# Performance work log

Measured on AMD Instinct MI355X. Metric: run time of the kernel, lower is better.

Reference implementation:

```python
import jax, jax.numpy as jnp
import numpy as np
import math

# ---- static config (mirrors init_kwargs) ----
B, CIN, COUT = 8, 32, 32
H, W = 256, 256
RADIUS_CUTOFF = 0.03
NR, NPHI = 6, 7               # kernel_shape = [6, 7] (anisotropic basis)
K = (NR - 1) * NPHI + 1       # 36 basis functions
EPS = 1e-5                    # InstanceNorm2d eps
NEG_SLOPE = 0.2


def _disco_psi(nh, nw, r_cutoff, nr, nphi):
    """Local DISCO filter basis on an equidistant [-1,1]^2 grid.
    Returns psi [K, P, P] (float32) and half-width p (P = 2p+1).
    Piecewise-linear hat functions in radius (nr rings incl. center) times
    hat functions in angle (nphi sectors), normalized and quadrature-weighted."""
    dy = 2.0 / nh
    dx = 2.0 / nw
    p = int(math.floor(r_cutoff / min(dx, dy)))
    off_y = (np.arange(-p, p + 1) * dy)[:, None]
    off_x = (np.arange(-p, p + 1) * dx)[None, :]
    r = np.sqrt(off_x ** 2 + off_y ** 2)                 # [P, P]
    phi = np.arctan2(off_y + 0 * off_x, off_x + 0 * off_y) % (2.0 * np.pi)
    dr = r_cutoff / nr
    dphi = 2.0 * np.pi / nphi
    ker = (nr - 1) * nphi + 1
    ik = np.arange(ker)[:, None, None]                   # [K,1,1]
    ir = ((ik - 1) // nphi + 1) * dr                     # ik=0 -> ring at r=0
    iphi = ((ik - 1) % nphi) * dphi
    norm = np.pi * (r_cutoff * nr / (nr + 1)) ** 2       # 2d normalization
    rv = np.clip(1.0 - np.abs(r[None] - ir) / dr, 0.0, None) * (r[None] <= r_cutoff)
    dphi_abs = np.abs(phi[None] - iphi)
    dphi_min = np.minimum(dphi_abs, 2.0 * np.pi - dphi_abs)
    pv = np.where(ik > 0, np.clip(1.0 - dphi_min / dphi, 0.0, None), 1.0)
    q = dx * dy                                          # quadrature weight
    psi = (rv * pv) * (q / norm)
    return jnp.asarray(psi, jnp.float32), p


def _upsample2x_bilinear_align_corners(x):
    """torch nn.Upsample(scale_factor=2, mode='bilinear', align_corners=True)."""
    b, c, hi, wi = x.shape
    ho, wo = 2 * hi, 2 * wi
    ys = jnp.linspace(0.0, hi - 1.0, ho)
    y0 = jnp.clip(jnp.floor(ys), 0, hi - 2).astype(jnp.int32)
    wy = (ys - y0.astype(ys.dtype))[None, None, :, None]
    x = x[:, :, y0, :] * (1.0 - wy) + x[:, :, y0 + 1, :] * wy
    xs = jnp.linspace(0.0, wi - 1.0, wo)
    x0 = jnp.clip(jnp.floor(xs), 0, wi - 2).astype(jnp.int32)
    wx = (xs - x0.astype(xs.dtype))[None, None, None, :]
    return x[:, :, :, x0] * (1.0 - wx) + x[:, :, :, x0 + 1] * wx


def setup_inputs() -> dict:
    key = jax.random.key(0)
    k1, k2 = jax.random.split(key)
    image = jax.random.normal(k1, (B, CIN, H, W), dtype=jnp.float32)
    # DISCO learnable weights: [out_ch, in_ch, kernel_size]
    scale = 1.0 / np.sqrt(CIN * K)
    weight = jax.random.normal(k2, (COUT, CIN, K), dtype=jnp.float32) * scale
    return {"image": image, "weight": weight}


def reference(image, weight):
    x = _upsample2x_bilinear_align_corners(image)
    # 2) equidistant DISCO conv: assemble dense kernel from basis, strided conv back to (H,W)
    psi, p = _disco_psi(2 * H, 2 * W, RADIUS_CUTOFF / 2.0, NR, NPHI)   # [K,P,P]
    kernel = jnp.einsum("oik,kyx->oiyx", weight, psi)                   # [O,I,P,P]
    y = jax.lax.conv_general_dilated(
        x, kernel, window_strides=(2, 2), padding=[(p, p), (p, p)],
        dimension_numbers=("NCHW", "OIHW", "NCHW"))                     # [B,O,H,W]
    # 3) InstanceNorm2d (no affine), biased variance over spatial dims
    mean = jnp.mean(y, axis=(2, 3), keepdims=True)
    var = jnp.var(y, axis=(2, 3), keepdims=True)
    y = (y - mean) * jax.lax.rsqrt(var + EPS)
    # 4) LeakyReLU(0.2)
    return jnp.where(y >= 0, y, NEG_SLOPE * y)
```

## Files before the change

### kernel.cpp

```cpp
#include <hip/hip_runtime.h>
#include <hip/hip_bf16.h>
#include <math.h>

#define B_     8
#define CIN_   32
#define COUT_  32
#define H_     256
#define W_     256
#define K_     36
#define P_     3
#define KW_    7
#define TAPS_  49
#define NPAIR_ 25
#define EPS_   1e-5f
#define SLOPE_ 0.2f

#define PART_OFF_F   25600
#define MEANRS_OFF_F 156672

#define IMG_PLANE_B   6736
#define IMG_ROW_B     336

#define XP_ROW   304
#define XO_BASE  11552

using short8_t  = __attribute__((ext_vector_type(8)))  short;
using f32x16_t  = __attribute__((ext_vector_type(16))) float;
using f32x4_t   = __attribute__((ext_vector_type(4)))  float;

__device__ inline ushort f32_to_bf16(float f) {
    unsigned int bits = __float_as_uint(f);
    unsigned int r = (bits + 0x7FFFu + ((bits >> 16) & 1u)) >> 16;
    return (ushort)r;
}

__host__ __device__ inline int pair_tap(int pi, int tt) {
    if (pi < 21) {
        const int ky = pi / 3, c = pi % 3;
        return ky * 7 + 2 * c + tt;
    }
    const int row = 2 * (pi - 21) + tt;
    return (row <= 6) ? (row * 7 + 6) : -1;
}

__global__ __launch_bounds__(256)
void build_kernel(const float* __restrict__ weight, ushort* __restrict__ kerB) {
    __shared__ float psi_s[2][K_];
    const int f  = blockIdx.x;
    const int pi = f % NPAIR_;
    const int oc = f / NPAIR_;
    const int tid = threadIdx.x;

    if (tid < 2 * K_) {
        const int tt = tid / K_;
        const int k  = tid - tt * K_;
        const int tap = pair_tap(pi, tt);
        float val = 0.f;
        if (tap >= 0) {
            const int ky = tap / 7;
            const int kx = tap % 7;
            const double dxy   = 2.0 / 512.0;
            const double rcut  = 0.015;
            const int    nr    = 6, nphi = 7;
            const double dr    = rcut / nr;
            const double dphi  = 2.0 * M_PI / nphi;
            const double norm  = M_PI * (rcut * nr / (nr + 1)) * (rcut * nr / (nr + 1));
            const double q     = dxy * dxy;
            const double offy = (double)(ky - P_) * dxy;
            const double offx = (double)(kx - P_) * dxy;
            const double r    = sqrt(offx * offx + offy * offy);
            double phi = atan2(offy, offx);
            if (phi < 0.0) phi += 2.0 * M_PI;
            double ir, iphi;
            if (k == 0) { ir = 0.0; iphi = 0.0; }
            else        { ir = (double)((k - 1) / nphi + 1) * dr;
                          iphi = (double)((k - 1) % nphi) * dphi; }
            double rv = 1.0 - fabs(r - ir) / dr;
            rv = rv > 0.0 ? rv : 0.0;
            if (r > rcut) rv = 0.0;
            double pv = 1.0;
            if (k > 0) {
                double da = fabs(phi - iphi);
                double dm = da < (2.0 * M_PI - da) ? da : (2.0 * M_PI - da);
                pv = 1.0 - dm / dphi;
                pv = pv > 0.0 ? pv : 0.0;
            }
            val = (float)(rv * pv * q / norm);
        }
        psi_s[tt][k] = val;
    }
    __syncthreads();

    for (int e = tid; e < 512; e += 256) {
        const int lane = e >> 3;
        const int j    = e & 7;
        const int gs   = lane >> 5;
        const int n    = lane & 31;
        float s = 0.f;
        if (pair_tap(pi, gs) >= 0) {
            const int ci = oc * 8 + j;
            const float* w = weight + (size_t)(n * CIN_ + ci) * K_;
            #pragma unroll
            for (int k = 0; k < K_; ++k) s = fmaf(w[k], psi_s[gs][k], s);
        }
        kerB[((size_t)f * 64 + lane) * 8 + j] = f32_to_bf16(s);
    }
}

__global__ __launch_bounds__(512, 8)
void conv_mfma(const float* __restrict__ image,
               const ushort* __restrict__ kerB,
               float* __restrict__ out,
               float* __restrict__ partials) {
    __shared__ float  Img_s[3368];
    __shared__ ushort Xup_s[11552];
    __shared__ float  wp[8][32][2];

    const int tid  = threadIdx.x;
    const int lane = tid & 63;
    const int w    = tid >> 6;
    const int j0 = blockIdx.x * 16;
    const int i0 = blockIdx.y * 16;
    const int b  = blockIdx.z;

    const int u0 = 2 * i0 - 3;
    const int v0 = 2 * j0 - 3;
    const int R0 = i0 - 2;
    const int C0 = j0 - 2;

    const int gs  = lane >> 5;
    const int tio = (lane & 31) >> 4;
    const int tj  = lane & 15;
    const int yb0 = 4 * w + 2 * tio;

    f32x16_t acc;
    #pragma unroll
    for (int q = 0; q < 16; ++q) acc[q] = 0.f;

    char* img_bytes = (char*)Img_s;
    char* xup_bytes = (char*)Xup_s;

    if (tid < 19) {
        const short8_t z = {0,0,0,0,0,0,0,0};
        *(short8_t*)(xup_bytes + 37 * XP_ROW + tid * 16) = z;
    }

    const float* imgb = image + (size_t)(b * CIN_) * (H_ * W_);

    for (int oc = 0; oc < 4; ++oc) {
        const float* img = imgb + (size_t)(oc * 8) * (H_ * W_);
        for (int e = tid; e < 800; e += 512) {
            const int p  = (e >= 400) ? 1 : 0;
            const int yx = e - p * 400;
            const int py = yx / 20, px = yx - py * 20;
            const int row = R0 + py, col = C0 + px;
            f32x4_t g = {0.f, 0.f, 0.f, 0.f};
            if ((unsigned)row < 256u && (unsigned)col < 256u) {
                const float* q = img + (size_t)p * 4 * (H_ * W_) + row * W_ + col;
                g[0] = q[0];
                g[1] = q[H_ * W_];
                g[2] = q[2 * (H_ * W_)];
                g[3] = q[3 * (H_ * W_)];
            }
            *(f32x4_t*)(img_bytes + p * IMG_PLANE_B + (py * 21 + px) * 16) = g;
        }
        __syncthreads();

        for (int e = tid; e < 703; e += 512) {
            const int y   = e / 19;
            const int xp  = e - 19 * y;
            const int x   = 2 * xp;
            const int ry  = y >> 1;
            const float wy =
                (float)((((y & 1) ? 510 : 255)) - (R0 + ry)) * (1.0f / 511.0f);
            const int Ax = C0 + xp;
            const float wx0 = (float)(255 - Ax) * (1.0f / 511.0f);
            const float wx1 = (float)(510 - Ax) * (1.0f / 511.0f);
            const bool oky = ((unsigned)(u0 + y) < 512u);
            const bool ok0 = oky && ((unsigned)(v0 + x) < 512u);
            const bool ok1 = oky && ((unsigned)(v0 + x + 1) < 512u) && (xp < 18);

            const char* lo = img_bytes + (ry * 21 + xp) * 16;
            const char* hi = lo + IMG_PLANE_B;
            const f32x4_t a00 = *(const f32x4_t*)(lo);
            const f32x4_t a01 = *(const f32x4_t*)(lo + 16);
            const f32x4_t a10 = *(const f32x4_t*)(lo + IMG_ROW_B);
            const f32x4_t a11 = *(const f32x4_t*)(lo + IMG_ROW_B + 16);
            const f32x4_t b00 = *(const f32x4_t*)(hi);
            const f32x4_t b01 = *(const f32x4_t*)(hi + 16);
            const f32x4_t b10 = *(const f32x4_t*)(hi + IMG_ROW_B);
            const f32x4_t b11 = *(const f32x4_t*)(hi + IMG_ROW_B + 16);

            const f32x4_t cA0 = a00 + wy * (a10 - a00);
            const f32x4_t cA1 = a01 + wy * (a11 - a01);
            const f32x4_t cB0 = b00 + wy * (b10 - b00);
            const f32x4_t cB1 = b01 + wy * (b11 - b01);

            {
                const f32x4_t va = cA0 + wx0 * (cA1 - cA0);
                const f32x4_t vb = cB0 + wx0 * (cB1 - cB0);
                __hip_bfloat162 h0 = __float22bfloat162_rn(make_float2(va[0], va[1]));
                __hip_bfloat162 h1 = __float22bfloat162_rn(make_float2(va[2], va[3]));
                __hip_bfloat162 h2 = __float22bfloat162_rn(make_float2(vb[0], vb[1]));
                __hip_bfloat162 h3 = __float22bfloat162_rn(make_float2(vb[2], vb[3]));
                union { short8_t s8; uint4 u4; } pk;
                pk.u4.x = ok0 ? *(unsigned int*)&h0 : 0u;
                pk.u4.y = ok0 ? *(unsigned int*)&h1 : 0u;
                pk.u4.z = ok0 ? *(unsigned int*)&h2 : 0u;
                pk.u4.w = ok0 ? *(unsigned int*)&h3 : 0u;
                *(short8_t*)(xup_bytes + y * XP_ROW + xp * 16) = pk.s8;
            }
            {
                const f32x4_t va = cA0 + wx1 * (cA1 - cA0);
                const f32x4_t vb = cB0 + wx1 * (cB1 - cB0);
                __hip_bfloat162 h0 = __float22bfloat162_rn(make_float2(va[0], va[1]));
                __hip_bfloat162 h1 = __float22bfloat162_rn(make_float2(va[2], va[3]));
                __hip_bfloat162 h2 = __float22bfloat162_rn(make_float2(vb[0], vb[1]));
                __hip_bfloat162 h3 = __float22bfloat162_rn(make_float2(vb[2], vb[3]));
                union { short8_t s8; uint4 u4; } pk;
                pk.u4.x = ok1 ? *(unsigned int*)&h0 : 0u;
                pk.u4.y = ok1 ? *(unsigned int*)&h1 : 0u;
                pk.u4.z = ok1 ? *(unsigned int*)&h2 : 0u;
                pk.u4.w = ok1 ? *(unsigned int*)&h3 : 0u;
                *(short8_t*)(xup_bytes + XO_BASE + y * XP_ROW + xp * 16) = pk.s8;
            }
        }
        __syncthreads();

        const ushort* kbp = kerB + ((size_t)(oc * NPAIR_) * 64 + lane) * 8;
        const int baseA = (gs ? XO_BASE : 0) + yb0 * XP_ROW + tj * 16;
        const int baseB = (yb0 + gs) * XP_ROW + (tj + 3) * 16;

        #pragma unroll
        for (int ky = 0; ky < KW_; ++ky) {
            short8_t bf0 = *(const short8_t*)(kbp + (size_t)((ky * 3 + 0) * 512));
            short8_t bf1 = *(const short8_t*)(kbp + (size_t)((ky * 3 + 1) * 512));
            short8_t bf2 = *(const short8_t*)(kbp + (size_t)((ky * 3 + 2) * 512));
            const int rbase = baseA + ky * XP_ROW;
            const short8_t a0 = *(const short8_t*)(xup_bytes + rbase);
            acc = __builtin_amdgcn_mfma_f32_32x32x16_bf16(a0, bf0, acc, 0, 0, 0);
            const short8_t a1 = *(const short8_t*)(xup_bytes + rbase + 16);
            acc = __builtin_amdgcn_mfma_f32_32x32x16_bf16(a1, bf1, acc, 0, 0, 0);
            const short8_t a2 = *(const short8_t*)(xup_bytes + rbase + 32);
            acc = __builtin_amdgcn_mfma_f32_32x32x16_bf16(a2, bf2, acc, 0, 0, 0);
        }
        #pragma unroll
        for (int q = 0; q < 4; ++q) {
            const short8_t bfq =
                *(const short8_t*)(kbp + (size_t)((21 + q) * 512));
            const short8_t aq =
                *(const short8_t*)(xup_bytes + baseB + q * (2 * XP_ROW));
            acc = __builtin_amdgcn_mfma_f32_32x32x16_bf16(aq, bfq, acc, 0, 0, 0);
        }
        __syncthreads();
    }

    const int n = lane & 31;
    float* op = out + (size_t)(b * COUT_ + n) * (H_ * W_);
    const int ibase = i0 + 2 * w;
    #pragma unroll
    for (int grp = 0; grp < 4; ++grp) {
        const int ti  = ibase + (grp >> 1);
        const int tjj = j0 + ((grp & 1) ? 8 : 0) + 4 * gs;
        f32x4_t s;
        s[0] = acc[grp * 4 + 0]; s[1] = acc[grp * 4 + 1];
        s[2] = acc[grp * 4 + 2]; s[3] = acc[grp * 4 + 3];
        *(f32x4_t*)(op + (size_t)ti * W_ + tjj) = s;
    }

    float s1 = 0.f, s2 = 0.f;
    #pragma unroll
    for (int q = 0; q < 16; ++q) { s1 += acc[q]; s2 = fmaf(acc[q], acc[q], s2); }
    s1 += __shfl_xor(s1, 32);
    s2 += __shfl_xor(s2, 32);
    if (lane < 32) { wp[w][lane][0] = s1; wp[w][lane][1] = s2; }
    __syncthreads();
    if (tid < 32) {
        float t1 = 0.f, t2 = 0.f;
        #pragma unroll
        for (int wv = 0; wv < 8; ++wv) { t1 += wp[wv][tid][0]; t2 += wp[wv][tid][1]; }
        const int tile = blockIdx.y * 16 + blockIdx.x;
        float2* pp = (float2*)partials;
        pp[((b * 32 + tid) << 8) | tile] = make_float2(t1, t2);
    }
}

__global__ __launch_bounds__(64)
void stats_kernel(const float* __restrict__ partials, float* __restrict__ meanrs) {
    const int bo = blockIdx.x;
    const int l  = threadIdx.x;
    const float2* pp = (const float2*)partials + ((size_t)bo << 8);
    float s1 = 0.f, s2 = 0.f;
    #pragma unroll
    for (int k = 0; k < 4; ++k) {
        const float2 p = pp[l + 64 * k];
        s1 += p.x; s2 += p.y;
    }
    #pragma unroll
    for (int off = 32; off > 0; off >>= 1) {
        s1 += __shfl_down(s1, off);
        s2 += __shfl_down(s2, off);
    }
    if (l == 0) {
        const float inv = 1.0f / 65536.0f;
        const float m   = s1 * inv;
        const float var = s2 * inv - m * m;
        ((float2*)meanrs)[bo] = make_float2(m, 1.0f / sqrtf(var + EPS_));
    }
}

__global__ __launch_bounds__(256)
void norm2_kernel(float* __restrict__ y, const float* __restrict__ meanrs) {
    const int blk = blockIdx.x;
    const int bo  = blk >> 6;
    const float2 mr = ((const float2*)meanrs)[bo];
    const float m  = mr.x;
    const float rs = mr.y;

    const int e = blk * 256 + threadIdx.x;
    float4 v = ((const float4*)y)[e];
    v.x = (v.x - m) * rs; v.x = v.x >= 0.f ? v.x : SLOPE_ * v.x;
    v.y = (v.y - m) * rs; v.y = v.y >= 0.f ? v.y : SLOPE_ * v.y;
    v.z = (v.z - m) * rs; v.z = v.z >= 0.f ? v.z : SLOPE_ * v.z;
    v.w = (v.w - m) * rs; v.w = v.w >= 0.f ? v.w : SLOPE_ * v.w;
    ((float4*)y)[e] = v;
}

extern "C" void kernel_launch(void* const* d_in, const int* in_sizes, int n_in,
                              void* d_out, int out_size, void* d_ws, size_t ws_size,
                              hipStream_t stream) {
    const float* image  = (const float*)d_in[0];
    const float* weight = (const float*)d_in[1];
    float*  out      = (float*)d_out;
    ushort* kerB     = (ushort*)d_ws;
    float*  partials = (float*)d_ws + PART_OFF_F;
    float*  meanrs   = (float*)d_ws + MEANRS_OFF_F;

    build_kernel<<<dim3(4 * NPAIR_), dim3(256), 0, stream>>>(weight, kerB);
    conv_mfma<<<dim3(16, 16, B_), dim3(512), 0, stream>>>(image, kerB, out, partials);
    stats_kernel<<<dim3(256), dim3(64), 0, stream>>>(partials, meanrs);
    norm2_kernel<<<dim3(16384), dim3(256), 0, stream>>>(out, meanrs);
}
```

Measured before the change: 116.8 us.

## Fuse image staging into upsample by reading global memory directly

Removes the shared-memory staging buffer for the input tile. Each thread now loads its four bilinear neighbours straight from global memory, with clamped indices, and writes bf16 upsampled values into the Xup buffer. The work is split per plane half, giving 1406 items instead of 703. This drops one barrier per channel group and the LDS footprint, which could raise occupancy. In exchange, each input pixel is fetched several times from global or L2 memory with scattered 4-byte loads.

```diff
diff --git a/kernel.cpp b/kernel.cpp
--- a/kernel.cpp
+++ b/kernel.cpp
@@ -17,9 +17,6 @@
 
 #define PART_OFF_F   25600
 #define MEANRS_OFF_F 156672
-
-#define IMG_PLANE_B   6736
-#define IMG_ROW_B     336
 
 #define XP_ROW   304
 #define XO_BASE  11552
@@ -112,7 +109,6 @@
                const ushort* __restrict__ kerB,
                float* __restrict__ out,
                float* __restrict__ partials) {
-    __shared__ float  Img_s[3368];
     __shared__ ushort Xup_s[11552];
     __shared__ float  wp[8][32][2];
 
@@ -137,93 +133,68 @@
     #pragma unroll
     for (int q = 0; q < 16; ++q) acc[q] = 0.f;
 
-    char* img_bytes = (char*)Img_s;
     char* xup_bytes = (char*)Xup_s;
 
     if (tid < 19) {
         const short8_t z = {0,0,0,0,0,0,0,0};
         *(short8_t*)(xup_bytes + 37 * XP_ROW + tid * 16) = z;
     }
+    __syncthreads();
 
     const float* imgb = image + (size_t)(b * CIN_) * (H_ * W_);
 
     for (int oc = 0; oc < 4; ++oc) {
-        const float* img = imgb + (size_t)(oc * 8) * (H_ * W_);
-        for (int e = tid; e < 800; e += 512) {
-            const int p  = (e >= 400) ? 1 : 0;
-            const int yx = e - p * 400;
-            const int py = yx / 20, px = yx - py * 20;
-            const int row = R0 + py, col = C0 + px;
-            f32x4_t g = {0.f, 0.f, 0.f, 0.f};
-            if ((unsigned)row < 256u && (unsigned)col < 256u) {
-                const float* q = img + (size_t)p * 4 * (H_ * W_) + row * W_ + col;
-                g[0] = q[0];
-                g[1] = q[H_ * W_];
-                g[2] = q[2 * (H_ * W_)];
-                g[3] = q[3 * (H_ * W_)];
+        for (int e = tid; e < 1406; e += 512) {
+            const int item = e >> 1;
+            const int p    = e & 1;
+            const int y    = item / 19;
+            const int xp   = item - 19 * y;
+            const int ry   = y >> 1;
+            const int r0   = R0 + ry;
+            const int c0   = C0 + xp;
+            const float wy  = (float)(((y & 1) ? 510 : 255) - r0) * (1.0f / 511.0f);
+            const float wx0 = (float)(255 - c0) * (1.0f / 511.0f);
+            const float wx1 = (float)(510 - c0) * (1.0f / 511.0f);
+            const bool oky = ((unsigned)(u0 + y) < 512u);
+            const bool ok0 = oky && ((unsigned)(v0 + 2 * xp) < 512u);
+            const bool ok1 = oky && ((unsigned)(v0 + 2 * xp + 1) < 512u) && (xp < 18);
+
+            const int r0c = r0 < 0 ? 0 : (r0 > 255 ? 255 : r0);
+            const int r1t = r0 + 1;
+            const int r1c = r1t < 0 ? 0 : (r1t > 255 ? 255 : r1t);
+            const int c0c = c0 < 0 ? 0 : (c0 > 255 ? 255 : c0);
+            const int c1t = c0 + 1;
+            const int c1c = c1t < 0 ? 0 : (c1t > 255 ? 255 : c1t);
+
+            const float* pl = imgb + (size_t)(oc * 8 + p * 4) * (H_ * W_);
+            const int o00 = r0c * W_ + c0c, o01 = r0c * W_ + c1c;
+            const int o10 = r1c * W_ + c0c, o11 = r1c * W_ + c1c;
+
+            float ve[4], vo[4];
+            #pragma unroll
+            for (int c = 0; c < 4; ++c) {
+                const float* q = pl + (size_t)c * (H_ * W_);
+                const float v00 = q[o00];
+                const float v01 = q[o01];
+                const float v10 = q[o10];
+                const float v11 = q[o11];
+                const float l0 = v00 + wy * (v10 - v00);
+                const float l1 = v01 + wy * (v11 - v01);
+                ve[c] = l0 + wx0 * (l1 - l0);
+                vo[c] = l0 + wx1 * (l1 - l0);
             }
-            *(f32x4_t*)(img_bytes + p * IMG_PLANE_B + (py * 21 + px) * 16) = g;
-        }
-        __syncthreads();
-
-        for (int e = tid; e < 703; e += 512) {
-            const int y   = e / 19;
-            const int xp  = e - 19 * y;
-            const int x   = 2 * xp;
-            const int ry  = y >> 1;
-            const float wy =
-                (float)((((y & 1) ? 510 : 255)) - (R0 + ry)) * (1.0f / 511.0f);
-            const int Ax = C0 + xp;
-            const float wx0 = (float)(255 - Ax) * (1.0f / 511.0f);
-            const float wx1 = (float)(510 - Ax) * (1.0f / 511.0f);
-            const bool oky = ((unsigned)(u0 + y) < 512u);
-            const bool ok0 = oky && ((unsigned)(v0 + x) < 512u);
-            const bool ok1 = oky && ((unsigned)(v0 + x + 1) < 512u) && (xp < 18);
-
-            const char* lo = img_bytes + (ry * 21 + xp) * 16;
-            const char* hi = lo + IMG_PLANE_B;
-            const f32x4_t a00 = *(const f32x4_t*)(lo);
-            const f32x4_t a01 = *(const f32x4_t*)(lo + 16);
-            const f32x4_t a10 = *(const f32x4_t*)(lo + IMG_ROW_B);
-            const f32x4_t a11 = *(const f32x4_t*)(lo + IMG_ROW_B + 16);
-            const f32x4_t b00 = *(const f32x4_t*)(hi);
-            const f32x4_t b01 = *(const f32x4_t*)(hi + 16);
-            const f32x4_t b10 = *(const f32x4_t*)(hi + IMG_ROW_B);
-            const f32x4_t b11 = *(const f32x4_t*)(hi + IMG_ROW_B + 16);
-
-            const f32x4_t cA0 = a00 + wy * (a10 - a00);
-            const f32x4_t cA1 = a01 + wy * (a11 - a01);
-            const f32x4_t cB0 = b00 + wy * (b10 - b00);
-            const f32x4_t cB1 = b01 + wy * (b11 - b01);
-
-            {
-                const f32x4_t va = cA0 + wx0 * (cA1 - cA0);
-                const f32x4_t vb = cB0 + wx0 * (cB1 - cB0);
-                __hip_bfloat162 h0 = __float22bfloat162_rn(make_float2(va[0], va[1]));
-                __hip_bfloat162 h1 = __float22bfloat162_rn(make_float2(va[2], va[3]));
-                __hip_bfloat162 h2 = __float22bfloat162_rn(make_float2(vb[0], vb[1]));
-                __hip_bfloat162 h3 = __float22bfloat162_rn(make_float2(vb[2], vb[3]));
-                union { short8_t s8; uint4 u4; } pk;
-                pk.u4.x = ok0 ? *(unsigned int*)&h0 : 0u;
-                pk.u4.y = ok0 ? *(unsigned int*)&h1 : 0u;
-                pk.u4.z = ok0 ? *(unsigned int*)&h2 : 0u;
-                pk.u4.w = ok0 ? *(unsigned int*)&h3 : 0u;
-                *(short8_t*)(xup_bytes + y * XP_ROW + xp * 16) = pk.s8;
-            }
-            {
-                const f32x4_t va = cA0 + wx1 * (cA1 - cA0);
-                const f32x4_t vb = cB0 + wx1 * (cB1 - cB0);
-                __hip_bfloat162 h0 = __float22bfloat162_rn(make_float2(va[0], va[1]));
-                __hip_bfloat162 h1 = __float22bfloat162_rn(make_float2(va[2], va[3]));
-                __hip_bfloat162 h2 = __float22bfloat162_rn(make_float2(vb[0], vb[1]));
-                __hip_bfloat162 h3 = __float22bfloat162_rn(make_float2(vb[2], vb[3]));
-                union { short8_t s8; uint4 u4; } pk;
-                pk.u4.x = ok1 ? *(unsigned int*)&h0 : 0u;
-                pk.u4.y = ok1 ? *(unsigned int*)&h1 : 0u;
-                pk.u4.z = ok1 ? *(unsigned int*)&h2 : 0u;
-                pk.u4.w = ok1 ? *(unsigned int*)&h3 : 0u;
-                *(short8_t*)(xup_bytes + XO_BASE + y * XP_ROW + xp * 16) = pk.s8;
-            }
+            __hip_bfloat162 he0 = __float22bfloat162_rn(make_float2(ve[0], ve[1]));
+            __hip_bfloat162 he1 = __float22bfloat162_rn(make_float2(ve[2], ve[3]));
+            __hip_bfloat162 ho0 = __float22bfloat162_rn(make_float2(vo[0], vo[1]));
+            __hip_bfloat162 ho1 = __float22bfloat162_rn(make_float2(vo[2], vo[3]));
+            uint2 pe, po;
+            pe.x = ok0 ? *(unsigned int*)&he0 : 0u;
+            pe.y = ok0 ? *(unsigned int*)&he1 : 0u;
+            po.x = ok1 ? *(unsigned int*)&ho0 : 0u;
+            po.y = ok1 ? *(unsigned int*)&ho1 : 0u;
+            const int sbase = y * XP_ROW + xp * 16 + p * 8;
+            *(uint2*)(xup_bytes + sbase) = pe;
+            *(uint2*)(xup_bytes + XO_BASE + sbase) = po;
         }
         __syncthreads();
 
```

Measured after the change: 180.1 us. 1.54x slower.
